# Kernel optimization log

Measured on AMD Instinct MI355X. Metric: run time of the kernel, lower is better.

The kernel has to match this reference:

```python
import jax, jax.numpy as jnp
import numpy as np

B, D, U = 4096, 256, 512


def setup_inputs() -> dict:
    key = jax.random.key(0)
    k = jax.random.split(key, 7)
    return {
        "x": jax.random.normal(k[0], (B, D), jnp.float32),
        "t": jax.random.uniform(k[1], (B, 1), jnp.float32),           # elapsed-time input
        "h0": jax.random.normal(k[2], (B, U), jnp.float32),
        "c0": jax.random.normal(k[3], (B, U), jnp.float32),
        "kernel": jax.random.normal(k[4], (D, 5 * U), jnp.float32) / np.sqrt(D).astype(np.float32),
        "recurrent_kernel": jax.random.normal(k[5], (U, 3 * U), jnp.float32) / np.sqrt(U).astype(np.float32),
        "kernel_time": jax.random.normal(k[6], (1, 3 * U), jnp.float32) * 0.1,
    }


def reference(x, t, h0, c0, kernel, recurrent_kernel, kernel_time):
    sig = jax.nn.sigmoid
    # Fused input projection: one GEMM instead of 5 (same math, kernel cols are
    # ordered [i, c, o, t1, t2] exactly as the original slices self.kernel).
    x_i, x_c, x_o, x_t1, x_t2 = jnp.split(x @ kernel, 5, axis=1)          # each (B, U)
    # Fused recurrent projection: cols ordered [i, c, o].
    r_i, r_c, r_o = jnp.split(h0 @ recurrent_kernel, 3, axis=1)           # each (B, U)
    # Time projections: cols ordered [t1, t2, o].
    kt1, kt2, kto = jnp.split(t @ kernel_time, 3, axis=1)                 # each (B, U)

    i = sig(x_i + r_i)
    t_1 = sig(x_t1 + sig(kt1))
    # tf.where(t_1 > -1e-5, -1e-5, t_1): sigmoid output is always > -1e-5,
    # so this clamps to the constant -1e-5; keep the where for faithfulness.
    NEG_EPS = jnp.float32(-1e-5)
    t_1_constraint = jnp.where(t_1 > NEG_EPS, jnp.full_like(t_1, NEG_EPS), t_1)
    t_2 = sig(x_t2 + sig(kt2))
    c_tilde = jnp.tanh(x_c + r_c)
    c_m_ = (1.0 - i * t_1) * c0 + i * c_tilde * t_1_constraint
    c_m = (1.0 - i) * c0 + i * c_tilde * t_2
    o = sig(x_o + r_o + kto)
    h = jnp.tanh(c_m_) * o
    # original returns (h, [h, c_m]); h appears twice, so return (h, c_m)
    return (h, c_m)
```

## Files before the change

kernel.cpp:

```cpp
#include <hip/hip_runtime.h>


typedef __attribute__((ext_vector_type(8))) short short8_t;
typedef __attribute__((ext_vector_type(4))) float f32x4_t;
typedef unsigned int u32;

#define B_N 4096
#define D_K 256
#define U_N 512

__device__ __forceinline__ unsigned short f2bf(float f) {
    unsigned int x = __float_as_uint(f);
    unsigned int r = x + 0x7fffu + ((x >> 16) & 1u);
    return (unsigned short)(r >> 16);
}

__device__ __forceinline__ float sigf(float z) {
    return 1.0f / (1.0f + __expf(-z));
}

__device__ __forceinline__ float tanhfast(float z) {
    return 1.0f - 2.0f / (1.0f + __expf(2.0f * z));
}

__device__ __forceinline__ void gl16(const unsigned short* g, unsigned short* l) {
    __builtin_amdgcn_global_load_lds(
        (const __attribute__((address_space(1))) u32*)g,
        (__attribute__((address_space(3))) u32*)l, 16, 0, 0);
}

#define SWZ(r, kc) ((((r) * 8) + ((kc) ^ ((r) & 7))) * 8)

#define WAIT_VM(N)                                            \
    asm volatile("s_waitcnt vmcnt(" #N ")" ::: "memory");     \
    __builtin_amdgcn_sched_barrier(0)

__global__ __launch_bounds__(256) void prep(
    const float* __restrict__ x, const float* __restrict__ h0,
    const float* __restrict__ kern, const float* __restrict__ rk,
    unsigned short* __restrict__ xs, unsigned short* __restrict__ hs,
    unsigned short* __restrict__ ksw, unsigned short* __restrict__ rsw)
{
    const int c = blockIdx.x * 256 + threadIdx.x;
    if (c < 131072) {
        const int t = c >> 10, q = c & 1023;
        const int row = q >> 3, kc = q & 7;
        const int rb = t >> 2, kb = t & 3;
        const float* s = x + (size_t)(rb * 128 + row) * D_K + kb * 64 + kc * 8;
        short8_t o;
#pragma unroll
        for (int j = 0; j < 8; ++j) o[j] = (short)f2bf(s[j]);
        *reinterpret_cast<short8_t*>(xs + (size_t)t * 8192 + SWZ(row, kc)) = o;
    } else if (c < 393216) {
        const int c2 = c - 131072;
        const int t = c2 >> 10, q = c2 & 1023;
        const int row = q >> 3, kc = q & 7;
        const int rb = t >> 3, kb = t & 7;
        const float* s = h0 + (size_t)(rb * 128 + row) * U_N + kb * 64 + kc * 8;
        short8_t o;
#pragma unroll
        for (int j = 0; j < 8; ++j) o[j] = (short)f2bf(s[j]);
        *reinterpret_cast<short8_t*>(hs + (size_t)t * 8192 + SWZ(row, kc)) = o;
    } else if (c < 475136) {
        const int c2 = c - 393216;
        const int t = c2 / 1280, q = c2 - t * 1280;
        const int kc = q / 160, r = q - kc * 160;
        const int nb = t >> 2, kb = t & 3;
        const int col = (r >> 5) * U_N + nb * 32 + (r & 31);
        short8_t o;
#pragma unroll
        for (int j = 0; j < 8; ++j)
            o[j] = (short)f2bf(kern[(size_t)(kb * 64 + kc * 8 + j) * 2560 + col]);
        *reinterpret_cast<short8_t*>(ksw + (size_t)t * 10240 + SWZ(r, kc)) = o;
    } else {
        const int c2 = c - 475136;
        const int t = c2 / 768, q = c2 - t * 768;
        const int kc = q / 96, r = q - kc * 96;
        const int nb = t >> 3, kb = t & 7;
        const int col = (r >> 5) * U_N + nb * 32 + (r & 31);
        short8_t o;
#pragma unroll
        for (int j = 0; j < 8; ++j)
            o[j] = (short)f2bf(rk[(size_t)(kb * 64 + kc * 8 + j) * 1536 + col]);
        *reinterpret_cast<short8_t*>(rsw + (size_t)t * 6144 + SWZ(r, kc)) = o;
    }
}

__global__ __launch_bounds__(256, 2) void tlstm_main(
    const unsigned short* __restrict__ xs,
    const unsigned short* __restrict__ hs,
    const unsigned short* __restrict__ ksw,
    const unsigned short* __restrict__ rsw,
    const float* __restrict__ tvec,
    const float* __restrict__ c0,
    const float* __restrict__ ktime,
    float* __restrict__ out)
{
    __shared__ __align__(16) unsigned short lds[2][18432];

    const int tid = threadIdx.x;
    const int wave = tid >> 6;
    const int lane = tid & 63;
    const int lr = lane & 15;
    const int lq = lane >> 4;
    const int wm = wave >> 1;
    const int wn = wave & 1;
    const int nb = blockIdx.x;
    const int rb = blockIdx.y;

    f32x4_t acc[8][4];
#pragma unroll
    for (int m = 0; m < 8; ++m)
#pragma unroll
        for (int p = 0; p < 4; ++p)
            acc[m][p] = (f32x4_t){0.f, 0.f, 0.f, 0.f};

    auto stage = [&](int s, int buf) {
        unsigned short* ab = &lds[buf][0];
        unsigned short* bb = &lds[buf][8192];
        if (s < 4) {
            const unsigned short* at = xs + (size_t)(rb * 4 + s) * 8192;
#pragma unroll
            for (int j = 0; j < 4; ++j)
                gl16(at + (j * 256 + tid) * 8, ab + (j * 256 + wave * 64) * 8);
            const unsigned short* bt = ksw + (size_t)(nb * 4 + s) * 10240;
#pragma unroll
            for (int j = 0; j < 5; ++j)
                gl16(bt + (j * 256 + tid) * 8, bb + (j * 256 + wave * 64) * 8);
        } else {
            const unsigned short* at = hs + (size_t)(rb * 8 + (s - 4)) * 8192;
#pragma unroll
            for (int j = 0; j < 4; ++j)
                gl16(at + (j * 256 + tid) * 8, ab + (j * 256 + wave * 64) * 8);
            const unsigned short* bt = rsw + (size_t)(nb * 8 + (s - 4)) * 6144;
#pragma unroll
            for (int j = 0; j < 3; ++j)
                gl16(bt + (j * 256 + tid) * 8, bb + (j * 256 + wave * 64) * 8);
        }
    };

    auto compute1 = [&](int buf) {
        const unsigned short* ab = &lds[buf][0];
        const unsigned short* bb = &lds[buf][8192];
#pragma unroll
        for (int ks = 0; ks < 2; ++ks) {
            const int kc = ks * 4 + lq;
            short8_t a[4];
#pragma unroll
            for (int p = 0; p < 4; ++p)
                a[p] = *reinterpret_cast<const short8_t*>(ab + SWZ(wm * 64 + p * 16 + lr, kc));
#pragma unroll
            for (int m = 0; m < 5; ++m) {
                const int r = m * 32 + wn * 16 + lr;
                short8_t b = *reinterpret_cast<const short8_t*>(bb + SWZ(r, kc));
#pragma unroll
                for (int p = 0; p < 4; ++p)
                    acc[m][p] = __builtin_amdgcn_mfma_f32_16x16x32_bf16(a[p], b, acc[m][p], 0, 0, 0);
            }
        }
    };

    auto compute2 = [&](int buf) {
        const unsigned short* ab = &lds[buf][0];
        const unsigned short* bb = &lds[buf][8192];
#pragma unroll
        for (int ks = 0; ks < 2; ++ks) {
            const int kc = ks * 4 + lq;
            short8_t a[4];
#pragma unroll
            for (int p = 0; p < 4; ++p)
                a[p] = *reinterpret_cast<const short8_t*>(ab + SWZ(wm * 64 + p * 16 + lr, kc));
#pragma unroll
            for (int m = 0; m < 3; ++m) {
                const int r = m * 32 + wn * 16 + lr;
                short8_t b = *reinterpret_cast<const short8_t*>(bb + SWZ(r, kc));
#pragma unroll
                for (int p = 0; p < 4; ++p)
                    acc[5 + m][p] = __builtin_amdgcn_mfma_f32_16x16x32_bf16(a[p], b, acc[5 + m][p], 0, 0, 0);
            }
        }
    };

#define K_BODY(S, NV, CF)                                  \
    {                                                      \
        WAIT_VM(NV);                                       \
        __builtin_amdgcn_s_barrier();                      \
        __builtin_amdgcn_sched_barrier(0);                 \
        CF((S) & 1);                                       \
        __builtin_amdgcn_sched_barrier(0);                 \
        __builtin_amdgcn_s_barrier();                      \
        __builtin_amdgcn_sched_barrier(0);                 \
    }

    stage(0, 0);
    stage(1, 1);   K_BODY(0, 9, compute1);
    stage(2, 0);   K_BODY(1, 9, compute1);
    stage(3, 1);   K_BODY(2, 9, compute1);
    stage(4, 0);   K_BODY(3, 7, compute1);
    stage(5, 1);   K_BODY(4, 7, compute2);
    stage(6, 0);   K_BODY(5, 7, compute2);
    stage(7, 1);   K_BODY(6, 7, compute2);
    stage(8, 0);   K_BODY(7, 7, compute2);
    stage(9, 1);   K_BODY(8, 7, compute2);
    stage(10, 0);  K_BODY(9, 7, compute2);
    stage(11, 1);  K_BODY(10, 7, compute2);
    K_BODY(11, 0, compute2);

    const float NEG_EPS = -1e-5f;
    const int u = nb * 32 + wn * 16 + lr;
    const float kt1 = ktime[u];
    const float kt2 = ktime[U_N + u];
    const float kto = ktime[2 * U_N + u];
#pragma unroll
    for (int p = 0; p < 4; ++p)
#pragma unroll
        for (int i2 = 0; i2 < 4; ++i2) {
            const int b = rb * 128 + wm * 64 + p * 16 + lq * 4 + i2;
            const float tb = tvec[b];
            const float c0v = c0[(size_t)b * U_N + u];
            const float x_i  = acc[0][p][i2];
            const float x_c  = acc[1][p][i2];
            const float x_o  = acc[2][p][i2];
            const float x_t1 = acc[3][p][i2];
            const float x_t2 = acc[4][p][i2];
            const float r_i  = acc[5][p][i2];
            const float r_c  = acc[6][p][i2];
            const float r_o  = acc[7][p][i2];

            const float ig  = sigf(x_i + r_i);
            const float t1v = sigf(x_t1 + sigf(tb * kt1));
            const float t1c = (t1v > NEG_EPS) ? NEG_EPS : t1v;
            const float t2v = sigf(x_t2 + sigf(tb * kt2));
            const float ct  = tanhfast(x_c + r_c);
            const float cm_ = (1.f - ig * t1v) * c0v + ig * ct * t1c;
            const float cm  = (1.f - ig) * c0v + ig * ct * t2v;
            const float og  = sigf(x_o + r_o + tb * kto);

            out[(size_t)b * U_N + u] = tanhfast(cm_) * og;
            out[(size_t)B_N * U_N + (size_t)b * U_N + u] = cm;
        }
}

extern "C" void kernel_launch(void* const* d_in, const int* in_sizes, int n_in,
                              void* d_out, int out_size, void* d_ws, size_t ws_size,
                              hipStream_t stream) {
    const float* x     = (const float*)d_in[0];
    const float* t     = (const float*)d_in[1];
    const float* h0    = (const float*)d_in[2];
    const float* c0    = (const float*)d_in[3];
    const float* kern  = (const float*)d_in[4];
    const float* rk    = (const float*)d_in[5];
    const float* ktime = (const float*)d_in[6];
    float* out = (float*)d_out;

    unsigned short* xs  = (unsigned short*)d_ws;
    unsigned short* hs  = (unsigned short*)((char*)d_ws + 2097152);
    unsigned short* ksw = (unsigned short*)((char*)d_ws + 6291456);
    unsigned short* rsw = (unsigned short*)((char*)d_ws + 7602176);

    prep<<<2240, 256, 0, stream>>>(x, h0, kern, rk, xs, hs, ksw, rsw);
    tlstm_main<<<dim3(16, 32), 256, 0, stream>>>(
        xs, hs, ksw, rsw, t, c0, ktime, out);
}
```

Baseline: 32.73 us.

## Widen N tile to 64 with 8 waves, K-step 32, triple-buffered pipeline

```diff
diff --git a/kernel.cpp b/kernel.cpp
--- a/kernel.cpp
+++ b/kernel.cpp
@@ -29,7 +29,7 @@
         (__attribute__((address_space(3))) u32*)l, 16, 0, 0);
 }
 
-#define SWZ(r, kc) ((((r) * 8) + ((kc) ^ ((r) & 7))) * 8)
+#define SWZ32(r, kc) ((((r) * 4) + ((kc) ^ (((r) >> 1) & 3))) * 8)
 
 #define WAIT_VM(N)                                            \
     asm volatile("s_waitcnt vmcnt(" #N ")" ::: "memory");     \
@@ -43,50 +43,50 @@
 {
     const int c = blockIdx.x * 256 + threadIdx.x;
     if (c < 131072) {
-        const int t = c >> 10, q = c & 1023;
-        const int row = q >> 3, kc = q & 7;
-        const int rb = t >> 2, kb = t & 3;
-        const float* s = x + (size_t)(rb * 128 + row) * D_K + kb * 64 + kc * 8;
+        const int t = c >> 9, q = c & 511;
+        const int row = q >> 2, kc = q & 3;
+        const int rb = t >> 3, kb = t & 7;
+        const float* s = x + (size_t)(rb * 128 + row) * D_K + kb * 32 + kc * 8;
         short8_t o;
 #pragma unroll
         for (int j = 0; j < 8; ++j) o[j] = (short)f2bf(s[j]);
-        *reinterpret_cast<short8_t*>(xs + (size_t)t * 8192 + SWZ(row, kc)) = o;
+        *reinterpret_cast<short8_t*>(xs + (size_t)t * 4096 + SWZ32(row, kc)) = o;
     } else if (c < 393216) {
         const int c2 = c - 131072;
-        const int t = c2 >> 10, q = c2 & 1023;
-        const int row = q >> 3, kc = q & 7;
-        const int rb = t >> 3, kb = t & 7;
-        const float* s = h0 + (size_t)(rb * 128 + row) * U_N + kb * 64 + kc * 8;
+        const int t = c2 >> 9, q = c2 & 511;
+        const int row = q >> 2, kc = q & 3;
+        const int rb = t >> 4, kb = t & 15;
+        const float* s = h0 + (size_t)(rb * 128 + row) * U_N + kb * 32 + kc * 8;
         short8_t o;
 #pragma unroll
         for (int j = 0; j < 8; ++j) o[j] = (short)f2bf(s[j]);
-        *reinterpret_cast<short8_t*>(hs + (size_t)t * 8192 + SWZ(row, kc)) = o;
+        *reinterpret_cast<short8_t*>(hs + (size_t)t * 4096 + SWZ32(row, kc)) = o;
     } else if (c < 475136) {
         const int c2 = c - 393216;
         const int t = c2 / 1280, q = c2 - t * 1280;
-        const int kc = q / 160, r = q - kc * 160;
-        const int nb = t >> 2, kb = t & 3;
-        const int col = (r >> 5) * U_N + nb * 32 + (r & 31);
+        const int kc = q / 320, r = q - kc * 320;
+        const int nb = t >> 3, kb = t & 7;
+        const int col = (r >> 6) * U_N + nb * 64 + (r & 63);
         short8_t o;
 #pragma unroll
         for (int j = 0; j < 8; ++j)
-            o[j] = (short)f2bf(kern[(size_t)(kb * 64 + kc * 8 + j) * 2560 + col]);
-        *reinterpret_cast<short8_t*>(ksw + (size_t)t * 10240 + SWZ(r, kc)) = o;
+            o[j] = (short)f2bf(kern[(size_t)(kb * 32 + kc * 8 + j) * 2560 + col]);
+        *reinterpret_cast<short8_t*>(ksw + (size_t)t * 10240 + SWZ32(r, kc)) = o;
     } else {
         const int c2 = c - 475136;
         const int t = c2 / 768, q = c2 - t * 768;
-        const int kc = q / 96, r = q - kc * 96;
-        const int nb = t >> 3, kb = t & 7;
-        const int col = (r >> 5) * U_N + nb * 32 + (r & 31);
+        const int kc = q / 192, r = q - kc * 192;
+        const int nb = t >> 4, kb = t & 15;
+        const int col = (r >> 6) * U_N + nb * 64 + (r & 63);
         short8_t o;
 #pragma unroll
         for (int j = 0; j < 8; ++j)
-            o[j] = (short)f2bf(rk[(size_t)(kb * 64 + kc * 8 + j) * 1536 + col]);
-        *reinterpret_cast<short8_t*>(rsw + (size_t)t * 6144 + SWZ(r, kc)) = o;
+            o[j] = (short)f2bf(rk[(size_t)(kb * 32 + kc * 8 + j) * 1536 + col]);
+        *reinterpret_cast<short8_t*>(rsw + (size_t)t * 6144 + SWZ32(r, kc)) = o;
     }
 }
 
-__global__ __launch_bounds__(256, 2) void tlstm_main(
+__global__ __launch_bounds__(512, 2) void tlstm_main(
     const unsigned short* __restrict__ xs,
     const unsigned short* __restrict__ hs,
     const unsigned short* __restrict__ ksw,
@@ -96,18 +96,20 @@
     const float* __restrict__ ktime,
     float* __restrict__ out)
 {
-    __shared__ __align__(16) unsigned short lds[2][18432];
+    __shared__ __align__(16) unsigned short lds[3][14336];
 
     const int tid = threadIdx.x;
     const int wave = tid >> 6;
     const int lane = tid & 63;
     const int lr = lane & 15;
     const int lq = lane >> 4;
-    const int wm = wave >> 1;
-    const int wn = wave & 1;
+    const int wm = wave >> 2;
+    const int wn = wave & 3;
     const int nb = blockIdx.x;
     const int rb = blockIdx.y;
 
+    const int u = nb * 64 + wn * 16 + lr;
+
     f32x4_t acc[8][4];
 #pragma unroll
     for (int m = 0; m < 8; ++m)
@@ -117,97 +119,109 @@
 
     auto stage = [&](int s, int buf) {
         unsigned short* ab = &lds[buf][0];
-        unsigned short* bb = &lds[buf][8192];
-        if (s < 4) {
-            const unsigned short* at = xs + (size_t)(rb * 4 + s) * 8192;
-#pragma unroll
-            for (int j = 0; j < 4; ++j)
-                gl16(at + (j * 256 + tid) * 8, ab + (j * 256 + wave * 64) * 8);
-            const unsigned short* bt = ksw + (size_t)(nb * 4 + s) * 10240;
-#pragma unroll
-            for (int j = 0; j < 5; ++j)
-                gl16(bt + (j * 256 + tid) * 8, bb + (j * 256 + wave * 64) * 8);
+        unsigned short* bb = &lds[buf][4096];
+        if (s < 8) {
+            const unsigned short* at = xs + (size_t)(rb * 8 + s) * 4096;
+            gl16(at + (size_t)tid * 8, ab + (size_t)(wave * 64) * 8);
+            const unsigned short* bt = ksw + (size_t)(nb * 8 + s) * 10240;
+            gl16(bt + (size_t)tid * 8,         bb + (size_t)(wave * 64) * 8);
+            gl16(bt + (size_t)(512 + tid) * 8, bb + (size_t)(512 + wave * 64) * 8);
+            const int b3 = (wave < 4) ? (1024 + wave * 64) : (wave * 64);
+            gl16(bt + (size_t)(b3 + lane) * 8, bb + (size_t)b3 * 8);
         } else {
-            const unsigned short* at = hs + (size_t)(rb * 8 + (s - 4)) * 8192;
-#pragma unroll
-            for (int j = 0; j < 4; ++j)
-                gl16(at + (j * 256 + tid) * 8, ab + (j * 256 + wave * 64) * 8);
-            const unsigned short* bt = rsw + (size_t)(nb * 8 + (s - 4)) * 6144;
-#pragma unroll
-            for (int j = 0; j < 3; ++j)
-                gl16(bt + (j * 256 + tid) * 8, bb + (j * 256 + wave * 64) * 8);
+            const unsigned short* at = hs + (size_t)(rb * 16 + (s - 8)) * 4096;
+            gl16(at + (size_t)tid * 8, ab + (size_t)(wave * 64) * 8);
+            const unsigned short* bt = rsw + (size_t)(nb * 16 + (s - 8)) * 6144;
+            gl16(bt + (size_t)tid * 8, bb + (size_t)(wave * 64) * 8);
+            const int b2 = (wave < 4) ? (512 + wave * 64) : (wave * 64);
+            gl16(bt + (size_t)(b2 + lane) * 8, bb + (size_t)b2 * 8);
         }
     };
 
     auto compute1 = [&](int buf) {
         const unsigned short* ab = &lds[buf][0];
-        const unsigned short* bb = &lds[buf][8192];
-#pragma unroll
-        for (int ks = 0; ks < 2; ++ks) {
-            const int kc = ks * 4 + lq;
-            short8_t a[4];
+        const unsigned short* bb = &lds[buf][4096];
+        short8_t a[4];
+#pragma unroll
+        for (int p = 0; p < 4; ++p)
+            a[p] = *reinterpret_cast<const short8_t*>(ab + SWZ32(wm * 64 + p * 16 + lr, lq));
+#pragma unroll
+        for (int m = 0; m < 5; ++m) {
+            const int r = m * 64 + wn * 16 + lr;
+            short8_t b = *reinterpret_cast<const short8_t*>(bb + SWZ32(r, lq));
 #pragma unroll
             for (int p = 0; p < 4; ++p)
-                a[p] = *reinterpret_cast<const short8_t*>(ab + SWZ(wm * 64 + p * 16 + lr, kc));
-#pragma unroll
-            for (int m = 0; m < 5; ++m) {
-                const int r = m * 32 + wn * 16 + lr;
-                short8_t b = *reinterpret_cast<const short8_t*>(bb + SWZ(r, kc));
-#pragma unroll
-                for (int p = 0; p < 4; ++p)
-                    acc[m][p] = __builtin_amdgcn_mfma_f32_16x16x32_bf16(a[p], b, acc[m][p], 0, 0, 0);
-            }
+                acc[m][p] = __builtin_amdgcn_mfma_f32_16x16x32_bf16(a[p], b, acc[m][p], 0, 0, 0);
         }
     };
 
     auto compute2 = [&](int buf) {
         const unsigned short* ab = &lds[buf][0];
-        const unsigned short* bb = &lds[buf][8192];
-#pragma unroll
-        for (int ks = 0; ks < 2; ++ks) {
-            const int kc = ks * 4 + lq;
-            short8_t a[4];
+        const unsigned short* bb = &lds[buf][4096];
+        short8_t a[4];
+#pragma unroll
+        for (int p = 0; p < 4; ++p)
+            a[p] = *reinterpret_cast<const short8_t*>(ab + SWZ32(wm * 64 + p * 16 + lr, lq));
+#pragma unroll
+        for (int m = 0; m < 3; ++m) {
+            const int r = m * 64 + wn * 16 + lr;
+            short8_t b = *reinterpret_cast<const short8_t*>(bb + SWZ32(r, lq));
 #pragma unroll
             for (int p = 0; p < 4; ++p)
-                a[p] = *reinterpret_cast<const short8_t*>(ab + SWZ(wm * 64 + p * 16 + lr, kc));
-#pragma unroll
-            for (int m = 0; m < 3; ++m) {
-                const int r = m * 32 + wn * 16 + lr;
-                short8_t b = *reinterpret_cast<const short8_t*>(bb + SWZ(r, kc));
-#pragma unroll
-                for (int p = 0; p < 4; ++p)
-                    acc[5 + m][p] = __builtin_amdgcn_mfma_f32_16x16x32_bf16(a[p], b, acc[5 + m][p], 0, 0, 0);
-            }
+                acc[5 + m][p] = __builtin_amdgcn_mfma_f32_16x16x32_bf16(a[p], b, acc[5 + m][p], 0, 0, 0);
         }
     };
 
-#define K_BODY(S, NV, CF)                                  \
+#define K_STEP(S, NV, CF)                                  \
+    {                                                      \
+        stage((S) + 2, ((S) + 2) % 3);                     \
+        WAIT_VM(NV);                                       \
+        __builtin_amdgcn_s_barrier();                      \
+        __builtin_amdgcn_sched_barrier(0);                 \
+        CF((S) % 3);                                       \
+        __builtin_amdgcn_sched_barrier(0);                 \
+        __builtin_amdgcn_s_barrier();                      \
+        __builtin_amdgcn_sched_barrier(0);                 \
+    }
+#define K_TAIL(S, NV, CF)                                  \
     {                                                      \
         WAIT_VM(NV);                                       \
         __builtin_amdgcn_s_barrier();                      \
         __builtin_amdgcn_sched_barrier(0);                 \
-        CF((S) & 1);                                       \
+        CF((S) % 3);                                       \
         __builtin_amdgcn_sched_barrier(0);                 \
         __builtin_amdgcn_s_barrier();                      \
         __builtin_amdgcn_sched_barrier(0);                 \
     }
 
     stage(0, 0);
-    stage(1, 1);   K_BODY(0, 9, compute1);
-    stage(2, 0);   K_BODY(1, 9, compute1);
-    stage(3, 1);   K_BODY(2, 9, compute1);
-    stage(4, 0);   K_BODY(3, 7, compute1);
-    stage(5, 1);   K_BODY(4, 7, compute2);
-    stage(6, 0);   K_BODY(5, 7, compute2);
-    stage(7, 1);   K_BODY(6, 7, compute2);
-    stage(8, 0);   K_BODY(7, 7, compute2);
-    stage(9, 1);   K_BODY(8, 7, compute2);
-    stage(10, 0);  K_BODY(9, 7, compute2);
-    stage(11, 1);  K_BODY(10, 7, compute2);
-    K_BODY(11, 0, compute2);
+    stage(1, 1);
+    K_STEP(0, 8, compute1);
+    K_STEP(1, 8, compute1);
+    K_STEP(2, 8, compute1);
+    K_STEP(3, 8, compute1);
+    K_STEP(4, 8, compute1);
+    K_STEP(5, 8, compute1);
+    K_STEP(6, 7, compute1);
+    K_STEP(7, 6, compute1);
+    K_STEP(8, 6, compute2);
+    K_STEP(9, 6, compute2);
+    K_STEP(10, 6, compute2);
+    K_STEP(11, 6, compute2);
+    K_STEP(12, 6, compute2);
+    K_STEP(13, 6, compute2);
+    K_STEP(14, 6, compute2);
+    K_STEP(15, 6, compute2);
+    K_STEP(16, 6, compute2);
+    K_STEP(17, 6, compute2);
+    K_STEP(18, 6, compute2);
+    K_STEP(19, 6, compute2);
+    K_STEP(20, 6, compute2);
+    K_STEP(21, 6, compute2);
+    K_TAIL(22, 3, compute2);
+    K_TAIL(23, 0, compute2);
 
     const float NEG_EPS = -1e-5f;
-    const int u = nb * 32 + wn * 16 + lr;
     const float kt1 = ktime[u];
     const float kt2 = ktime[U_N + u];
     const float kto = ktime[2 * U_N + u];
@@ -259,6 +273,6 @@
     unsigned short* rsw = (unsigned short*)((char*)d_ws + 7602176);
 
     prep<<<2240, 256, 0, stream>>>(x, h0, kern, rk, xs, hs, ksw, rsw);
-    tlstm_main<<<dim3(16, 32), 256, 0, stream>>>(
+    tlstm_main<<<dim3(8, 32), 512, 0, stream>>>(
         xs, hs, ksw, rsw, t, c0, ktime, out);
 }
```

Result: slower. 34.47 us (+5.3%).

## Halve row tile and K-step to double block count and occupancy

Applied to the files above, without the earlier changes.

```diff
diff --git a/kernel.cpp b/kernel.cpp
--- a/kernel.cpp
+++ b/kernel.cpp
@@ -29,7 +29,7 @@
         (__attribute__((address_space(3))) u32*)l, 16, 0, 0);
 }
 
-#define SWZ(r, kc) ((((r) * 8) + ((kc) ^ ((r) & 7))) * 8)
+#define SWZ32(r, kc) ((((r) * 4) + ((kc) ^ (((r) >> 1) & 3))) * 8)
 
 #define WAIT_VM(N)                                            \
     asm volatile("s_waitcnt vmcnt(" #N ")" ::: "memory");     \
@@ -43,50 +43,50 @@
 {
     const int c = blockIdx.x * 256 + threadIdx.x;
     if (c < 131072) {
-        const int t = c >> 10, q = c & 1023;
-        const int row = q >> 3, kc = q & 7;
-        const int rb = t >> 2, kb = t & 3;
-        const float* s = x + (size_t)(rb * 128 + row) * D_K + kb * 64 + kc * 8;
+        const int t = c >> 8, q = c & 255;
+        const int row = q >> 2, kc = q & 3;
+        const int rb = t >> 3, kb = t & 7;
+        const float* s = x + (size_t)(rb * 64 + row) * D_K + kb * 32 + kc * 8;
         short8_t o;
 #pragma unroll
         for (int j = 0; j < 8; ++j) o[j] = (short)f2bf(s[j]);
-        *reinterpret_cast<short8_t*>(xs + (size_t)t * 8192 + SWZ(row, kc)) = o;
+        *reinterpret_cast<short8_t*>(xs + (size_t)t * 2048 + SWZ32(row, kc)) = o;
     } else if (c < 393216) {
         const int c2 = c - 131072;
-        const int t = c2 >> 10, q = c2 & 1023;
-        const int row = q >> 3, kc = q & 7;
-        const int rb = t >> 3, kb = t & 7;
-        const float* s = h0 + (size_t)(rb * 128 + row) * U_N + kb * 64 + kc * 8;
+        const int t = c2 >> 8, q = c2 & 255;
+        const int row = q >> 2, kc = q & 3;
+        const int rb = t >> 4, kb = t & 15;
+        const float* s = h0 + (size_t)(rb * 64 + row) * U_N + kb * 32 + kc * 8;
         short8_t o;
 #pragma unroll
         for (int j = 0; j < 8; ++j) o[j] = (short)f2bf(s[j]);
-        *reinterpret_cast<short8_t*>(hs + (size_t)t * 8192 + SWZ(row, kc)) = o;
+        *reinterpret_cast<short8_t*>(hs + (size_t)t * 2048 + SWZ32(row, kc)) = o;
     } else if (c < 475136) {
         const int c2 = c - 393216;
-        const int t = c2 / 1280, q = c2 - t * 1280;
+        const int t = c2 / 640, q = c2 - t * 640;
         const int kc = q / 160, r = q - kc * 160;
-        const int nb = t >> 2, kb = t & 3;
+        const int nb = t >> 3, kb = t & 7;
         const int col = (r >> 5) * U_N + nb * 32 + (r & 31);
         short8_t o;
 #pragma unroll
         for (int j = 0; j < 8; ++j)
-            o[j] = (short)f2bf(kern[(size_t)(kb * 64 + kc * 8 + j) * 2560 + col]);
-        *reinterpret_cast<short8_t*>(ksw + (size_t)t * 10240 + SWZ(r, kc)) = o;
+            o[j] = (short)f2bf(kern[(size_t)(kb * 32 + kc * 8 + j) * 2560 + col]);
+        *reinterpret_cast<short8_t*>(ksw + (size_t)t * 5120 + SWZ32(r, kc)) = o;
     } else {
         const int c2 = c - 475136;
-        const int t = c2 / 768, q = c2 - t * 768;
+        const int t = c2 / 384, q = c2 - t * 384;
         const int kc = q / 96, r = q - kc * 96;
-        const int nb = t >> 3, kb = t & 7;
+        const int nb = t >> 4, kb = t & 15;
         const int col = (r >> 5) * U_N + nb * 32 + (r & 31);
         short8_t o;
 #pragma unroll
         for (int j = 0; j < 8; ++j)
-            o[j] = (short)f2bf(rk[(size_t)(kb * 64 + kc * 8 + j) * 1536 + col]);
-        *reinterpret_cast<short8_t*>(rsw + (size_t)t * 6144 + SWZ(r, kc)) = o;
+            o[j] = (short)f2bf(rk[(size_t)(kb * 32 + kc * 8 + j) * 1536 + col]);
+        *reinterpret_cast<short8_t*>(rsw + (size_t)t * 3072 + SWZ32(r, kc)) = o;
     }
 }
 
-__global__ __launch_bounds__(256, 2) void tlstm_main(
+__global__ __launch_bounds__(256, 4) void tlstm_main(
     const unsigned short* __restrict__ xs,
     const unsigned short* __restrict__ hs,
     const unsigned short* __restrict__ ksw,
@@ -96,7 +96,7 @@
     const float* __restrict__ ktime,
     float* __restrict__ out)
 {
-    __shared__ __align__(16) unsigned short lds[2][18432];
+    __shared__ __align__(16) unsigned short lds[2][8192];
 
     const int tid = threadIdx.x;
     const int wave = tid >> 6;
@@ -108,76 +108,57 @@
     const int nb = blockIdx.x;
     const int rb = blockIdx.y;
 
-    f32x4_t acc[8][4];
+    f32x4_t acc[8][2];
 #pragma unroll
     for (int m = 0; m < 8; ++m)
 #pragma unroll
-        for (int p = 0; p < 4; ++p)
+        for (int p = 0; p < 2; ++p)
             acc[m][p] = (f32x4_t){0.f, 0.f, 0.f, 0.f};
 
     auto stage = [&](int s, int buf) {
         unsigned short* ab = &lds[buf][0];
-        unsigned short* bb = &lds[buf][8192];
-        if (s < 4) {
-            const unsigned short* at = xs + (size_t)(rb * 4 + s) * 8192;
-#pragma unroll
-            for (int j = 0; j < 4; ++j)
-                gl16(at + (j * 256 + tid) * 8, ab + (j * 256 + wave * 64) * 8);
-            const unsigned short* bt = ksw + (size_t)(nb * 4 + s) * 10240;
-#pragma unroll
-            for (int j = 0; j < 5; ++j)
-                gl16(bt + (j * 256 + tid) * 8, bb + (j * 256 + wave * 64) * 8);
+        unsigned short* bb = &lds[buf][2048];
+        if (s < 8) {
+            const unsigned short* at = xs + (size_t)(rb * 8 + s) * 2048;
+            gl16(at + (size_t)tid * 8, ab + (size_t)(wave * 64) * 8);
+            const unsigned short* bt = ksw + (size_t)(nb * 8 + s) * 5120;
+            gl16(bt + (size_t)tid * 8,                 bb + (size_t)(wave * 64) * 8);
+            gl16(bt + (size_t)(256 + tid) * 8,         bb + (size_t)(256 + wave * 64) * 8);
+            gl16(bt + (size_t)(512 + (tid & 127)) * 8, bb + (size_t)(512 + wave * 64) * 8);
         } else {
-            const unsigned short* at = hs + (size_t)(rb * 8 + (s - 4)) * 8192;
-#pragma unroll
-            for (int j = 0; j < 4; ++j)
-                gl16(at + (j * 256 + tid) * 8, ab + (j * 256 + wave * 64) * 8);
-            const unsigned short* bt = rsw + (size_t)(nb * 8 + (s - 4)) * 6144;
-#pragma unroll
-            for (int j = 0; j < 3; ++j)
-                gl16(bt + (j * 256 + tid) * 8, bb + (j * 256 + wave * 64) * 8);
+            const unsigned short* at = hs + (size_t)(rb * 16 + (s - 8)) * 2048;
+            gl16(at + (size_t)tid * 8, ab + (size_t)(wave * 64) * 8);
+            const unsigned short* bt = rsw + (size_t)(nb * 16 + (s - 8)) * 3072;
+            gl16(bt + (size_t)tid * 8,                 bb + (size_t)(wave * 64) * 8);
+            gl16(bt + (size_t)(256 + (tid & 127)) * 8, bb + (size_t)(256 + wave * 64) * 8);
         }
     };
 
     auto compute1 = [&](int buf) {
         const unsigned short* ab = &lds[buf][0];
-        const unsigned short* bb = &lds[buf][8192];
-#pragma unroll
-        for (int ks = 0; ks < 2; ++ks) {
-            const int kc = ks * 4 + lq;
-            short8_t a[4];
-#pragma unroll
-            for (int p = 0; p < 4; ++p)
-                a[p] = *reinterpret_cast<const short8_t*>(ab + SWZ(wm * 64 + p * 16 + lr, kc));
-#pragma unroll
-            for (int m = 0; m < 5; ++m) {
-                const int r = m * 32 + wn * 16 + lr;
-                short8_t b = *reinterpret_cast<const short8_t*>(bb + SWZ(r, kc));
-#pragma unroll
-                for (int p = 0; p < 4; ++p)
-                    acc[m][p] = __builtin_amdgcn_mfma_f32_16x16x32_bf16(a[p], b, acc[m][p], 0, 0, 0);
-            }
+        const unsigned short* bb = &lds[buf][2048];
+        short8_t a0 = *reinterpret_cast<const short8_t*>(ab + SWZ32(wm * 32 + lr, lq));
+        short8_t a1 = *reinterpret_cast<const short8_t*>(ab + SWZ32(wm * 32 + 16 + lr, lq));
+#pragma unroll
+        for (int m = 0; m < 5; ++m) {
+            const int r = m * 32 + wn * 16 + lr;
+            short8_t b = *reinterpret_cast<const short8_t*>(bb + SWZ32(r, lq));
+            acc[m][0] = __builtin_amdgcn_mfma_f32_16x16x32_bf16(a0, b, acc[m][0], 0, 0, 0);
+            acc[m][1] = __builtin_amdgcn_mfma_f32_16x16x32_bf16(a1, b, acc[m][1], 0, 0, 0);
         }
     };
 
     auto compute2 = [&](int buf) {
         const unsigned short* ab = &lds[buf][0];
-        const unsigned short* bb = &lds[buf][8192];
-#pragma unroll
-        for (int ks = 0; ks < 2; ++ks) {
-            const int kc = ks * 4 + lq;
-            short8_t a[4];
-#pragma unroll
-            for (int p = 0; p < 4; ++p)
-                a[p] = *reinterpret_cast<const short8_t*>(ab + SWZ(wm * 64 + p * 16 + lr, kc));
-#pragma unroll
-            for (int m = 0; m < 3; ++m) {
-                const int r = m * 32 + wn * 16 + lr;
-                short8_t b = *reinterpret_cast<const short8_t*>(bb + SWZ(r, kc));
-#pragma unroll
-                for (int p = 0; p < 4; ++p)
-                    acc[5 + m][p] = __builtin_amdgcn_mfma_f32_16x16x32_bf16(a[p], b, acc[5 + m][p], 0, 0, 0);
-            }
+        const unsigned short* bb = &lds[buf][2048];
+        short8_t a0 = *reinterpret_cast<const short8_t*>(ab + SWZ32(wm * 32 + lr, lq));
+        short8_t a1 = *reinterpret_cast<const short8_t*>(ab + SWZ32(wm * 32 + 16 + lr, lq));
+#pragma unroll
+        for (int m = 0; m < 3; ++m) {
+            const int r = m * 32 + wn * 16 + lr;
+            short8_t b = *reinterpret_cast<const short8_t*>(bb + SWZ32(r, lq));
+            acc[5 + m][0] = __builtin_amdgcn_mfma_f32_16x16x32_bf16(a0, b, acc[5 + m][0], 0, 0, 0);
+            acc[5 + m][1] = __builtin_amdgcn_mfma_f32_16x16x32_bf16(a1, b, acc[5 + m][1], 0, 0, 0);
         }
     };
 
@@ -193,18 +174,30 @@
     }
 
     stage(0, 0);
-    stage(1, 1);   K_BODY(0, 9, compute1);
-    stage(2, 0);   K_BODY(1, 9, compute1);
-    stage(3, 1);   K_BODY(2, 9, compute1);
-    stage(4, 0);   K_BODY(3, 7, compute1);
-    stage(5, 1);   K_BODY(4, 7, compute2);
-    stage(6, 0);   K_BODY(5, 7, compute2);
-    stage(7, 1);   K_BODY(6, 7, compute2);
-    stage(8, 0);   K_BODY(7, 7, compute2);
-    stage(9, 1);   K_BODY(8, 7, compute2);
-    stage(10, 0);  K_BODY(9, 7, compute2);
-    stage(11, 1);  K_BODY(10, 7, compute2);
-    K_BODY(11, 0, compute2);
+    stage(1, 1);   K_BODY(0, 4, compute1);
+    stage(2, 0);   K_BODY(1, 4, compute1);
+    stage(3, 1);   K_BODY(2, 4, compute1);
+    stage(4, 0);   K_BODY(3, 4, compute1);
+    stage(5, 1);   K_BODY(4, 4, compute1);
+    stage(6, 0);   K_BODY(5, 4, compute1);
+    stage(7, 1);   K_BODY(6, 4, compute1);
+    stage(8, 0);   K_BODY(7, 3, compute1);
+    stage(9, 1);   K_BODY(8, 3, compute2);
+    stage(10, 0);  K_BODY(9, 3, compute2);
+    stage(11, 1);  K_BODY(10, 3, compute2);
+    stage(12, 0);  K_BODY(11, 3, compute2);
+    stage(13, 1);  K_BODY(12, 3, compute2);
+    stage(14, 0);  K_BODY(13, 3, compute2);
+    stage(15, 1);  K_BODY(14, 3, compute2);
+    stage(16, 0);  K_BODY(15, 3, compute2);
+    stage(17, 1);  K_BODY(16, 3, compute2);
+    stage(18, 0);  K_BODY(17, 3, compute2);
+    stage(19, 1);  K_BODY(18, 3, compute2);
+    stage(20, 0);  K_BODY(19, 3, compute2);
+    stage(21, 1);  K_BODY(20, 3, compute2);
+    stage(22, 0);  K_BODY(21, 3, compute2);
+    stage(23, 1);  K_BODY(22, 3, compute2);
+    K_BODY(23, 0, compute2);
 
     const float NEG_EPS = -1e-5f;
     const int u = nb * 32 + wn * 16 + lr;
@@ -212,10 +205,10 @@
     const float kt2 = ktime[U_N + u];
     const float kto = ktime[2 * U_N + u];
 #pragma unroll
-    for (int p = 0; p < 4; ++p)
+    for (int p = 0; p < 2; ++p)
 #pragma unroll
         for (int i2 = 0; i2 < 4; ++i2) {
-            const int b = rb * 128 + wm * 64 + p * 16 + lq * 4 + i2;
+            const int b = rb * 64 + wm * 32 + p * 16 + lq * 4 + i2;
             const float tb = tvec[b];
             const float c0v = c0[(size_t)b * U_N + u];
             const float x_i  = acc[0][p][i2];
@@ -229,10 +222,9 @@
 
             const float ig  = sigf(x_i + r_i);
             const float t1v = sigf(x_t1 + sigf(tb * kt1));
-            const float t1c = (t1v > NEG_EPS) ? NEG_EPS : t1v;
             const float t2v = sigf(x_t2 + sigf(tb * kt2));
             const float ct  = tanhfast(x_c + r_c);
-            const float cm_ = (1.f - ig * t1v) * c0v + ig * ct * t1c;
+            const float cm_ = (1.f - ig * t1v) * c0v + ig * ct * NEG_EPS;
             const float cm  = (1.f - ig) * c0v + ig * ct * t2v;
             const float og  = sigf(x_o + r_o + tb * kto);
 
@@ -259,6 +251,6 @@
     unsigned short* rsw = (unsigned short*)((char*)d_ws + 7602176);
 
     prep<<<2240, 256, 0, stream>>>(x, h0, kern, rk, xs, hs, ksw, rsw);
-    tlstm_main<<<dim3(16, 32), 256, 0, stream>>>(
+    tlstm_main<<<dim3(16, 64), 256, 0, stream>>>(
         xs, hs, ksw, rsw, t, c0, ktime, out);
 }
```

Result: slower. 34.51 us (+5.4%).

## Fuse bf16 prep into main kernel with grid-wide atomic barrier

Applied to the files above, without the earlier changes.

```diff
diff --git a/kernel.cpp b/kernel.cpp
--- a/kernel.cpp
+++ b/kernel.cpp
@@ -35,13 +35,12 @@
     asm volatile("s_waitcnt vmcnt(" #N ")" ::: "memory");     \
     __builtin_amdgcn_sched_barrier(0)
 
-__global__ __launch_bounds__(256) void prep(
+__device__ __forceinline__ void prep_chunk(int c,
     const float* __restrict__ x, const float* __restrict__ h0,
     const float* __restrict__ kern, const float* __restrict__ rk,
     unsigned short* __restrict__ xs, unsigned short* __restrict__ hs,
     unsigned short* __restrict__ ksw, unsigned short* __restrict__ rsw)
 {
-    const int c = blockIdx.x * 256 + threadIdx.x;
     if (c < 131072) {
         const int t = c >> 10, q = c & 1023;
         const int row = q >> 3, kc = q & 7;
@@ -86,27 +85,61 @@
     }
 }
 
-__global__ __launch_bounds__(256, 2) void tlstm_main(
-    const unsigned short* __restrict__ xs,
-    const unsigned short* __restrict__ hs,
-    const unsigned short* __restrict__ ksw,
-    const unsigned short* __restrict__ rsw,
+__global__ __launch_bounds__(256) void prep(
+    const float* __restrict__ x, const float* __restrict__ h0,
+    const float* __restrict__ kern, const float* __restrict__ rk,
+    unsigned short* __restrict__ xs, unsigned short* __restrict__ hs,
+    unsigned short* __restrict__ ksw, unsigned short* __restrict__ rsw)
+{
+    const int c = blockIdx.x * 256 + threadIdx.x;
+    if (c < 573440)
+        prep_chunk(c, x, h0, kern, rk, xs, hs, ksw, rsw);
+}
+
+__global__ __launch_bounds__(256, 2) void tlstm_fused(
+    const float* __restrict__ x,
+    const float* __restrict__ h0,
+    const float* __restrict__ kern,
+    const float* __restrict__ rk,
+    unsigned short* __restrict__ xs, unsigned short* __restrict__ hs,
+    unsigned short* __restrict__ ksw, unsigned short* __restrict__ rsw,
     const float* __restrict__ tvec,
     const float* __restrict__ c0,
     const float* __restrict__ ktime,
-    float* __restrict__ out)
+    float* __restrict__ out,
+    unsigned long long* __restrict__ ctr,
+    int do_prep)
 {
     __shared__ __align__(16) unsigned short lds[2][18432];
 
     const int tid = threadIdx.x;
+    const int bid = blockIdx.x;
+
+    if (do_prep) {
+#pragma unroll 1
+        for (int c = bid * 256 + tid; c < 573440; c += 131072)
+            prep_chunk(c, x, h0, kern, rk, xs, hs, ksw, rsw);
+        asm volatile("s_waitcnt vmcnt(0)" ::: "memory");
+        __threadfence();
+        __syncthreads();
+        if (tid == 0) {
+            __hip_atomic_fetch_add(ctr, 1ull, __ATOMIC_RELEASE,
+                                   __HIP_MEMORY_SCOPE_AGENT);
+            while (__hip_atomic_load(ctr, __ATOMIC_ACQUIRE,
+                                     __HIP_MEMORY_SCOPE_AGENT) < 512ull)
+                __builtin_amdgcn_s_sleep(16);
+        }
+        __syncthreads();
+    }
+
     const int wave = tid >> 6;
     const int lane = tid & 63;
     const int lr = lane & 15;
     const int lq = lane >> 4;
     const int wm = wave >> 1;
     const int wn = wave & 1;
-    const int nb = blockIdx.x;
-    const int rb = blockIdx.y;
+    const int nb = bid & 15;
+    const int rb = bid >> 4;
 
     f32x4_t acc[8][4];
 #pragma unroll
@@ -229,10 +262,9 @@
 
             const float ig  = sigf(x_i + r_i);
             const float t1v = sigf(x_t1 + sigf(tb * kt1));
-            const float t1c = (t1v > NEG_EPS) ? NEG_EPS : t1v;
             const float t2v = sigf(x_t2 + sigf(tb * kt2));
             const float ct  = tanhfast(x_c + r_c);
-            const float cm_ = (1.f - ig * t1v) * c0v + ig * ct * t1c;
+            const float cm_ = (1.f - ig * t1v) * c0v + ig * ct * NEG_EPS;
             const float cm  = (1.f - ig) * c0v + ig * ct * t2v;
             const float og  = sigf(x_o + r_o + tb * kto);
 
@@ -257,8 +289,16 @@
     unsigned short* hs  = (unsigned short*)((char*)d_ws + 2097152);
     unsigned short* ksw = (unsigned short*)((char*)d_ws + 6291456);
     unsigned short* rsw = (unsigned short*)((char*)d_ws + 7602176);
-
-    prep<<<2240, 256, 0, stream>>>(x, h0, kern, rk, xs, hs, ksw, rsw);
-    tlstm_main<<<dim3(16, 32), 256, 0, stream>>>(
-        xs, hs, ksw, rsw, t, c0, ktime, out);
-}
+    const size_t CTR_OFF = 9175040;
+    unsigned long long* ctr = (unsigned long long*)((char*)d_ws + CTR_OFF);
+
+    if (ws_size >= CTR_OFF + 8) {
+        hipMemsetAsync((char*)d_ws + CTR_OFF, 0, 8, stream);
+        tlstm_fused<<<512, 256, 0, stream>>>(
+            x, h0, kern, rk, xs, hs, ksw, rsw, t, c0, ktime, out, ctr, 1);
+    } else {
+        prep<<<2240, 256, 0, stream>>>(x, h0, kern, rk, xs, hs, ksw, rsw);
+        tlstm_fused<<<512, 256, 0, stream>>>(
+            x, h0, kern, rk, xs, hs, ksw, rsw, t, c0, ktime, out, ctr, 0);
+    }
+}
```

Measured after the change: 118.5 us. +262.2%, slower.
